# Kernel tuning notes

Measured on AMD Instinct MI355X. Metric: run time of the kernel, lower is better.

The kernel has to match this reference:

```python
import jax, jax.numpy as jnp
import numpy as np
from jax import lax

GAMMA = 1.5
ALPHA = 0.4
RADIUS = 2            # cv2 d=5 -> radius 2
SIGMA_COLOR = 0.05
SIGMA_SPACE = 50.0
BN_EPS = 1e-5


def setup_inputs() -> dict:
    key = jax.random.key(0)
    ks = jax.random.split(key, 6)
    B, C, H, W, F, L = 8, 1, 256, 256, 64, 15
    x = jax.random.normal(ks[0], (B, C, H, W), dtype=jnp.float32)
    w_init = jax.random.normal(ks[1], (F, C, 3, 3), dtype=jnp.float32) * 0.05
    w_body = jax.random.normal(ks[2], (L, F, F, 3, 3), dtype=jnp.float32) * 0.05
    bn_gamma = jnp.ones((L, F), dtype=jnp.float32) + 0.1 * jax.random.normal(ks[3], (L, F), dtype=jnp.float32)
    bn_beta = 0.1 * jax.random.normal(ks[4], (L, F), dtype=jnp.float32)
    w_final = jax.random.normal(ks[5], (C, F, 3, 3), dtype=jnp.float32) * 0.05
    return {"x": x, "w_init": w_init, "w_body": w_body,
            "bn_gamma": bn_gamma, "bn_beta": bn_beta, "w_final": w_final}


def _bilateral(img):
    # img: [B, H, W]; 5x5 bilateral filter, reflect-101 borders (cv2 default)
    r = RADIUS
    H, W = img.shape[1], img.shape[2]
    p = jnp.pad(img, ((0, 0), (r, r), (r, r)), mode='reflect')
    inv2sc = 1.0 / (2.0 * SIGMA_COLOR * SIGMA_COLOR)
    inv2ss = 1.0 / (2.0 * SIGMA_SPACE * SIGMA_SPACE)
    num = jnp.zeros_like(img)
    den = jnp.zeros_like(img)
    for dy in range(-r, r + 1):
        for dx in range(-r, r + 1):
            nb = p[:, dy + r:dy + r + H, dx + r:dx + r + W]
            sw = np.exp(-(dy * dy + dx * dx) * (1.0 / (2.0 * SIGMA_SPACE ** 2)))
            w = sw * jnp.exp(-(nb - img) ** 2 * inv2sc)
            num = num + w * nb
            den = den + w
    return num / den


def _preprocess(x):
    # x: [B, 1, H, W] in [-1, 1] nominal range
    xn = jnp.clip((x + 1.0) * 0.5, 1e-6, 1.0)
    img = xn[:, 0]                              # [B, H, W]
    blended = (1.0 - ALPHA) * img + ALPHA * jnp.power(img, GAMMA)
    return _bilateral(blended)[:, None]         # [B, 1, H, W]


def _conv(h, w):
    return lax.conv_general_dilated(h, w, (1, 1), 'SAME',
                                    dimension_numbers=('NCHW', 'OIHW', 'NCHW'))


def _dncnn(x_pre, w_init, w_body, bn_gamma, bn_beta, w_final):
    h = jax.nn.relu(_conv(x_pre, w_init))

    def body(h, params):
        w, g, b = params
        h = jax.nn.relu(_conv(h, w))
        mean = jnp.mean(h, axis=(0, 2, 3))
        var = jnp.var(h, axis=(0, 2, 3))
        h = (h - mean[None, :, None, None]) * jax.lax.rsqrt(var + BN_EPS)[None, :, None, None]
        h = h * g[None, :, None, None] + b[None, :, None, None]
        h = jax.nn.relu(h)
        return h, None

    h, _ = lax.scan(body, h, (w_body, bn_gamma, bn_beta))
    noise = _conv(h, w_final)
    return x_pre - noise


def reference(x, w_init, w_body, bn_gamma, bn_beta, w_final):
    x_pre = _preprocess(x)
    return _dncnn(x_pre, w_init, w_body, bn_gamma, bn_beta, w_final)
```

## Files before the change

kernel.cpp:

```cpp
#include <hip/hip_runtime.h>
#include <math.h>

#define B_   8
#define CH   64
#define H_   256
#define W_   256
#define NPIX (H_*W_)
#define NIMG (B_*NPIX)
#define NBLK 4096
#define PS   16

typedef short bf16x8 __attribute__((ext_vector_type(8)));
typedef float f32x4  __attribute__((ext_vector_type(4)));

__device__ float g_stats[256];
__device__ float g_part[128 * NBLK];
__device__ __align__(16) short g_wpk[15 * 18 * 4 * 64 * 16];

__device__ __forceinline__ int refl(int i) {
    if (i < 0)    return -i;
    if (i >= 256) return 510 - i;
    return i;
}
__device__ __forceinline__ float prep1(float v) {
    float xn = fminf(fmaxf((v + 1.0f) * 0.5f, 1e-6f), 1.0f);
    return 0.6f * xn + 0.4f * xn * sqrtf(xn);
}
__device__ __forceinline__ unsigned short bf16_rne(float f) {
    union { float f; unsigned u; } v; v.f = f;
    unsigned r = v.u + 0x7FFFu + ((v.u >> 16) & 1u);
    return (unsigned short)(r >> 16);
}
__device__ __forceinline__ float bf16_f(unsigned short h) {
    union { float f; unsigned u; } v; v.u = ((unsigned)h) << 16;
    return v.f;
}
__device__ __forceinline__ unsigned cvt_pk_bf16(float a, float b) {
    unsigned r;
    asm volatile("v_cvt_pk_bf16_f32 %0, %1, %2" : "=v"(r) : "v"(a), "v"(b));
    return r;
}
__device__ __forceinline__ void bar_lds() {
    asm volatile("s_waitcnt lgkmcnt(0)" ::: "memory");
    __builtin_amdgcn_s_barrier();
}

__global__ void init_ab_kernel() {
    int c = threadIdx.x;
    g_stats[128 + c] = 1.0f;
    g_stats[192 + c] = 0.0f;
}

__global__ void prepack_kernel(const float* __restrict__ w_body) {
    int idx = blockIdx.x * 256 + threadIdx.x;
    if (idx >= 15*18*4*64) return;
    int lane = idx & 63;
    int m    = (idx >> 6) & 3;
    int r2   = idx >> 8;
    int l    = r2 / 18;
    int s    = r2 - l * 18;
    int t  = s >> 1;
    int oc = m * 16 + (lane & 15);
    int icb = (s & 1) * 32 + (lane >> 4) * 8;
    union { short s[8]; int4 v; } uh, ul;
    #pragma unroll
    for (int j = 0; j < 8; ++j) {
        float w = w_body[(((size_t)l * 64 + oc) * 64 + (icb + j)) * 9 + t];
        unsigned short h = bf16_rne(w);
        unsigned short lo = bf16_rne(w - bf16_f(h));
        uh.s[j] = (short)h;
        ul.s[j] = (short)lo;
    }
    int4* dst = (int4*)(g_wpk + (size_t)idx * 16);
    dst[0] = uh.v;
    dst[1] = ul.v;
}

__global__ __launch_bounds__(256) void conv_init_kernel(
    const float* __restrict__ x, const float* __restrict__ wi,
    float* __restrict__ h)
{
    __shared__ float s_bl[14][38];
    __shared__ float s_xp[10][34];
    __shared__ float s_w[64 * 12];
    int bx = blockIdx.x, by = blockIdx.y, b = blockIdx.z;
    int tid = threadIdx.x;
    const float* xb = x + b * NPIX;

    for (int i = tid; i < 14*38; i += 256) {
        int r = i / 38, c = i - r * 38;
        int gy = refl(by * 8 + r - 3), gx = refl(bx * 32 + c - 3);
        s_bl[r][c] = prep1(xb[gy * W_ + gx]);
    }
    for (int i = tid; i < 576; i += 256) {
        int oc = i / 9, t = i - oc * 9;
        s_w[oc * 12 + t] = wi[i];
    }
    __syncthreads();

    for (int i = tid; i < 10*34; i += 256) {
        int r = i / 34, c = i - r * 34;
        int gy = by * 8 + r - 1, gx = bx * 32 + c - 1;
        float v = 0.f;
        if (gy >= 0 && gy < H_ && gx >= 0 && gx < W_) {
            float ctr = s_bl[r + 2][c + 2];
            float num = 0.f, den = 0.f;
            #pragma unroll
            for (int dy = -2; dy <= 2; ++dy)
                #pragma unroll
                for (int dx = -2; dx <= 2; ++dx) {
                    float nb = s_bl[r + 2 + dy][c + 2 + dx];
                    float d  = nb - ctr;
                    float wgt = expf(-(float)(dy*dy + dx*dx) * 2e-4f - d * d * 200.0f);
                    num += wgt * nb;
                    den += wgt;
                }
            v = num / den;
        }
        s_xp[r][c] = v;
    }
    __syncthreads();

    int px = tid & 31, py = tid >> 5;
    float v[9];
    #pragma unroll
    for (int dr = 0; dr < 3; ++dr)
        #pragma unroll
        for (int dc = 0; dc < 3; ++dc)
            v[dr*3+dc] = s_xp[py + dr][px + dc];

    float acc[64];
    #pragma unroll
    for (int oc = 0; oc < 64; ++oc) {
        f32x4 w0 = *(const f32x4*)&s_w[oc * 12];
        f32x4 w1 = *(const f32x4*)&s_w[oc * 12 + 4];
        float w8 = s_w[oc * 12 + 8];
        float a = w0[0]*v[0] + w0[1]*v[1] + w0[2]*v[2] + w0[3]*v[3];
        a += w1[0]*v[4] + w1[1]*v[5] + w1[2]*v[6] + w1[3]*v[7];
        a = fmaf(w8, v[8], a);
        acc[oc] = fmaxf(a, 0.f);
    }

    int gy = by * 8 + py, gx = bx * 32 + px;
    float* outp = h + ((size_t)(b * NPIX + gy * W_ + gx)) * 64;
    #pragma unroll
    for (int c4 = 0; c4 < 16; ++c4) {
        float4 o = make_float4(acc[4*c4], acc[4*c4+1], acc[4*c4+2], acc[4*c4+3]);
        *reinterpret_cast<float4*>(outp + 4*c4) = o;
    }
}

__global__ __launch_bounds__(256, 4) void conv_body_mfma(
    const float* __restrict__ hin, int l, float* __restrict__ hout)
{
    __shared__ unsigned s_hi[180 * PS];
    __shared__ unsigned s_lo[180 * PS];

    int tid  = threadIdx.x;
    int lane = tid & 63;
    int wv   = tid >> 6;

    int bid = blockIdx.x;
    int swz = (bid & 7) * 512 + (bid >> 3);
    int bx = swz & 15;
    int by = (swz >> 4) & 31;
    int b  = swz >> 9;

    const float* ab = &g_stats[128];
    int q   = tid & 7;
    int c0  = q * 4;
    int pr0 = tid >> 3;

    f32x4 acc[4][2];
    #pragma unroll
    for (int m = 0; m < 4; ++m)
        #pragma unroll
        for (int n = 0; n < 2; ++n)
            acc[m][n] = (f32x4){0.f, 0.f, 0.f, 0.f};

    auto split_store = [&](int p, float v0, float v1, float v2, float v3) {
        unsigned hh0 = cvt_pk_bf16(v0, v1);
        unsigned hh1 = cvt_pk_bf16(v2, v3);
        float f0 = __uint_as_float(hh0 << 16);
        float f1 = __uint_as_float(hh0 & 0xffff0000u);
        float f2 = __uint_as_float(hh1 << 16);
        float f3 = __uint_as_float(hh1 & 0xffff0000u);
        unsigned ll0 = cvt_pk_bf16(v0 - f0, v1 - f1);
        unsigned ll1 = cvt_pk_bf16(v2 - f2, v3 - f3);
        *(uint2*)&s_hi[p * PS + 2*q] = make_uint2(hh0, hh1);
        *(uint2*)&s_lo[p * PS + 2*q] = make_uint2(ll0, ll1);
    };

    auto stage_safe = [&](int chunk) {
        float4 a4 = *(const float4*)&ab[chunk * 32 + c0];
        float4 b4 = *(const float4*)&ab[64 + chunk * 32 + c0];
        #pragma unroll
        for (int k = 0; k < 6; ++k) {
            int p = k * 32 + pr0;
            if (p < 180) {
                int y = p / 18, xx = p - y * 18;
                int gy = by * 8 + y - 1, gx = bx * 16 + xx - 1;
                bool inb = (gy >= 0 && gy < H_ && gx >= 0 && gx < W_);
                const float4* src = (const float4*)(
                    hin + ((size_t)(b * NPIX + (inb ? gy * W_ + gx : 0))) * 64 + chunk * 32 + c0);
                float4 v = *src;
                float v0 = inb ? fmaxf(fmaf(v.x, a4.x, b4.x), 0.f) : 0.f;
                float v1 = inb ? fmaxf(fmaf(v.y, a4.y, b4.y), 0.f) : 0.f;
                float v2 = inb ? fmaxf(fmaf(v.z, a4.z, b4.z), 0.f) : 0.f;
                float v3 = inb ? fmaxf(fmaf(v.w, a4.w, b4.w), 0.f) : 0.f;
                split_store(p, v0, v1, v2, v3);
            }
        }
    };

    auto stage_fast = [&](int chunk) {
        float4 a4 = *(const float4*)&ab[chunk * 32 + c0];
        float4 b4 = *(const float4*)&ab[64 + chunk * 32 + c0];
        const float* hbase = hin
            + ((size_t)(b * NPIX + (by * 8 - 1) * W_ + (bx * 16 - 1))) * 64
            + chunk * 32 + c0;
        #pragma unroll
        for (int k = 0; k < 6; ++k) {
            int p = k * 32 + pr0;
            if (p < 180) {
                int y = p / 18, xx = p - y * 18;
                float4 v = *(const float4*)(hbase + ((size_t)(y * W_ + xx)) * 64);
                float v0 = fmaxf(fmaf(v.x, a4.x, b4.x), 0.f);
                float v1 = fmaxf(fmaf(v.y, a4.y, b4.y), 0.f);
                float v2 = fmaxf(fmaf(v.z, a4.z, b4.z), 0.f);
                float v3 = fmaxf(fmaf(v.w, a4.w, b4.w), 0.f);
                split_store(p, v0, v1, v2, v3);
            }
        }
    };

    bool interior = (bx >= 1 && bx <= 14 && by >= 1 && by <= 30);

    auto compute_chunk = [&](int chunk) {
        __builtin_amdgcn_s_setprio(1);
        #pragma unroll
        for (int t = 0; t < 9; ++t) {
            int s = 2 * t + chunk;
            const short* wb = g_wpk + ((size_t)(((l * 18 + s) * 4) * 64 + lane)) * 16;
            bf16x8 a_hi[4], a_lo[4];
            #pragma unroll
            for (int m = 0; m < 4; ++m) {
                const short* pw = wb + (size_t)m * 1024;
                a_hi[m] = *(const bf16x8*)(pw);
                a_lo[m] = *(const bf16x8*)(pw + 8);
            }
            int dr = t / 3, dc = t - dr * 3;
            #pragma unroll
            for (int n = 0; n < 2; ++n) {
                int y = 2 * wv + n + dr;
                int p = y * 18 + dc + (lane & 15);
                int woff = p * PS + (lane >> 4) * 4;
                bf16x8 b_hi = *(const bf16x8*)&s_hi[woff];
                bf16x8 b_lo = *(const bf16x8*)&s_lo[woff];
                #pragma unroll
                for (int m = 0; m < 4; ++m) {
                    acc[m][n] = __builtin_amdgcn_mfma_f32_16x16x32_bf16(a_hi[m], b_hi, acc[m][n], 0, 0, 0);
                    acc[m][n] = __builtin_amdgcn_mfma_f32_16x16x32_bf16(a_hi[m], b_lo, acc[m][n], 0, 0, 0);
                    acc[m][n] = __builtin_amdgcn_mfma_f32_16x16x32_bf16(a_lo[m], b_hi, acc[m][n], 0, 0, 0);
                }
            }
        }
        __builtin_amdgcn_s_setprio(0);
    };

    int ck0 = (bid >> 8) & 1;
    if (interior) stage_fast(ck0); else stage_safe(ck0);
    bar_lds();
    compute_chunk(ck0);
    bar_lds();
    if (interior) stage_fast(ck0 ^ 1); else stage_safe(ck0 ^ 1);
    bar_lds();
    compute_chunk(ck0 ^ 1);

    bar_lds();
    float* s_red = (float*)s_hi;

    int q4  = lane >> 4;
    int gxs = bx * 16 + (lane & 15);
    float ps1[4][4], ps2[4][4];
    #pragma unroll
    for (int m = 0; m < 4; ++m)
        #pragma unroll
        for (int r = 0; r < 4; ++r) { ps1[m][r] = 0.f; ps2[m][r] = 0.f; }

    #pragma unroll
    for (int n = 0; n < 2; ++n) {
        int gy = by * 8 + 2 * wv + n;
        float* op = hout + ((size_t)(b * NPIX + gy * W_ + gxs)) * 64 + q4 * 4;
        #pragma unroll
        for (int m = 0; m < 4; ++m) {
            float a0 = fmaxf(acc[m][n][0], 0.f);
            float a1 = fmaxf(acc[m][n][1], 0.f);
            float a2 = fmaxf(acc[m][n][2], 0.f);
            float a3 = fmaxf(acc[m][n][3], 0.f);
            *reinterpret_cast<float4*>(op + m * 16) = make_float4(a0, a1, a2, a3);
            ps1[m][0] += a0; ps1[m][1] += a1; ps1[m][2] += a2; ps1[m][3] += a3;
            ps2[m][0] += a0*a0; ps2[m][1] += a1*a1; ps2[m][2] += a2*a2; ps2[m][3] += a3*a3;
        }
    }
    #pragma unroll
    for (int m = 0; m < 4; ++m) {
        #pragma unroll
        for (int r = 0; r < 4; ++r) {
            float a = ps1[m][r], s = ps2[m][r];
            #pragma unroll
            for (int off = 1; off < 16; off <<= 1) {
                a += __shfl_xor(a, off);
                s += __shfl_xor(s, off);
            }
            if ((lane & 15) == 0) {
                int oc = m * 16 + q4 * 4 + r;
                s_red[(wv * 64 + oc) * 2]     = a;
                s_red[(wv * 64 + oc) * 2 + 1] = s;
            }
        }
    }
    __syncthreads();
    if (tid < 128) {
        float v = s_red[tid] + s_red[128 + tid] + s_red[256 + tid] + s_red[384 + tid];
        g_part[(size_t)tid * NBLK + bid] = v;
    }
}

__global__ __launch_bounds__(256) void bn_finalize_kernel(
    const float* __restrict__ gamma, const float* __restrict__ beta)
{
    __shared__ float s[8];
    int c = blockIdx.x;
    int t = threadIdx.x;
    const float* p1 = g_part + (size_t)(2 * c) * NBLK;
    const float* p2 = g_part + (size_t)(2 * c + 1) * NBLK;
    float s1 = 0.f, s2 = 0.f;
    for (int i = t; i < NBLK; i += 256) { s1 += p1[i]; s2 += p2[i]; }
    #pragma unroll
    for (int off = 32; off >= 1; off >>= 1) {
        s1 += __shfl_xor(s1, off);
        s2 += __shfl_xor(s2, off);
    }
    int lane = t & 63, w = t >> 6;
    if (lane == 0) { s[w * 2] = s1; s[w * 2 + 1] = s2; }
    __syncthreads();
    if (t == 0) {
        float sum = s[0] + s[2] + s[4] + s[6];
        float sq  = s[1] + s[3] + s[5] + s[7];
        const float invN = 1.0f / (float)NIMG;
        float mean = sum * invN;
        float var  = sq * invN - mean * mean;
        float a = gamma[c] / sqrtf(var + 1e-5f);
        g_stats[128 + c] = a;
        g_stats[192 + c] = beta[c] - mean * a;
    }
}

__global__ __launch_bounds__(256) void conv_final_kernel(
    const float* __restrict__ hin, const float* __restrict__ wf,
    const float* __restrict__ x, float* __restrict__ out)
{
    __shared__ float s_in[324 * 36];
    __shared__ float s_bl[20][21];
    __shared__ float s_w[64 * 12];
    int bx = blockIdx.x, by = blockIdx.y, b = blockIdx.z;
    int tid = threadIdx.x;
    const float* xb = x + b * NPIX;
    const float* ab = &g_stats[128];

    for (int i = tid; i < 20*20; i += 256) {
        int r = i / 20, c = i - r * 20;
        int gy = refl(by * 16 + r - 2), gx = refl(bx * 16 + c - 2);
        s_bl[r][c] = prep1(xb[gy * W_ + gx]);
    }
    for (int i = tid; i < 576; i += 256) {
        int ic = i / 9, t = i - ic * 9;
        s_w[ic * 12 + t] = wf[i];
    }
    __syncthreads();

    int px = tid & 15, py = tid >> 4;
    float ctr = s_bl[py + 2][px + 2];
    float num = 0.f, den = 0.f;
    #pragma unroll
    for (int dy = -2; dy <= 2; ++dy)
        #pragma unroll
        for (int dx = -2; dx <= 2; ++dx) {
            float nb = s_bl[py + 2 + dy][px + 2 + dx];
            float d  = nb - ctr;
            float wgt = expf(-(float)(dy*dy + dx*dx) * 2e-4f - d * d * 200.0f);
            num += wgt * nb;
            den += wgt;
        }
    float xpre = num / den;

    int q   = tid & 7;
    int c0  = q * 4;
    int pr0 = tid >> 3;
    float acc = 0.f;

    for (int chunk = 0; chunk < 2; ++chunk) {
        __syncthreads();
        float4 a4 = *(const float4*)&ab[chunk * 32 + c0];
        float4 b4 = *(const float4*)&ab[64 + chunk * 32 + c0];
        #pragma unroll
        for (int k = 0; k < 11; ++k) {
            int p = k * 32 + pr0;
            if (p < 324) {
                int y = p / 18, xx = p - y * 18;
                int gy = by * 16 + y - 1, gx = bx * 16 + xx - 1;
                bool inb = (gy >= 0 && gy < H_ && gx >= 0 && gx < W_);
                const float4* src = (const float4*)(
                    hin + ((size_t)(b * NPIX + (inb ? gy * W_ + gx : 0))) * 64 + chunk * 32 + c0);
                float4 v = *src;
                float4 o;
                o.x = inb ? fmaxf(fmaf(v.x, a4.x, b4.x), 0.f) : 0.f;
                o.y = inb ? fmaxf(fmaf(v.y, a4.y, b4.y), 0.f) : 0.f;
                o.z = inb ? fmaxf(fmaf(v.z, a4.z, b4.z), 0.f) : 0.f;
                o.w = inb ? fmaxf(fmaf(v.w, a4.w, b4.w), 0.f) : 0.f;
                *(float4*)&s_in[p * 36 + 4*q] = o;
            }
        }
        __syncthreads();

        #pragma unroll
        for (int u = 0; u < 8; ++u) {
            f32x4 wreg[4][3];
            #pragma unroll
            for (int e = 0; e < 4; ++e)
                #pragma unroll
                for (int g = 0; g < 3; ++g)
                    wreg[e][g] = *(const f32x4*)&s_w[(chunk * 32 + u * 4 + e) * 12 + g * 4];
            #pragma unroll
            for (int t = 0; t < 9; ++t) {
                int dr = t / 3, dc = t - dr * 3;
                const float4 hv = *(const float4*)&s_in[((py + dr) * 18 + px + dc) * 36 + 4 * u];
                acc = fmaf(hv.x, wreg[0][t >> 2][t & 3], acc);
                acc = fmaf(hv.y, wreg[1][t >> 2][t & 3], acc);
                acc = fmaf(hv.z, wreg[2][t >> 2][t & 3], acc);
                acc = fmaf(hv.w, wreg[3][t >> 2][t & 3], acc);
            }
        }
    }

    int gy = by * 16 + py, gx = bx * 16 + px;
    out[b * NPIX + gy * W_ + gx] = xpre - acc;
}

extern "C" void kernel_launch(void* const* d_in, const int* in_sizes, int n_in,
                              void* d_out, int out_size, void* d_ws, size_t ws_size,
                              hipStream_t stream)
{
    const float* x        = (const float*)d_in[0];
    const float* w_init   = (const float*)d_in[1];
    const float* w_body   = (const float*)d_in[2];
    const float* bn_gamma = (const float*)d_in[3];
    const float* bn_beta  = (const float*)d_in[4];
    const float* w_final  = (const float*)d_in[5];
    float* out = (float*)d_out;

    char* wsb = (char*)d_ws;
    float* hA = (float*)wsb;
    float* hB = (float*)(wsb + 134217728ULL);

    init_ab_kernel <<<1, 64, 0, stream>>>();
    prepack_kernel <<<270, 256, 0, stream>>>(w_body);
    conv_init_kernel<<<dim3(8, 32, 8), 256, 0, stream>>>(x, w_init, hA);

    float* cur = hA;
    float* nxt = hB;
    for (int l = 0; l < 15; ++l) {
        conv_body_mfma<<<NBLK, 256, 0, stream>>>(cur, l, nxt);
        bn_finalize_kernel<<<64, 256, 0, stream>>>(bn_gamma + l * 64, bn_beta + l * 64);
        float* tp = cur; cur = nxt; nxt = tp;
    }
    conv_final_kernel<<<dim3(16, 16, 8), 256, 0, stream>>>(cur, w_final, x, out);
}
```

Before: 2.139 ms.

## Switch body conv MFMA from 16x16x32 to 32x32x16 tiles

```diff
diff --git a/kernel.cpp b/kernel.cpp
--- a/kernel.cpp
+++ b/kernel.cpp
@@ -12,10 +12,11 @@
 
 typedef short bf16x8 __attribute__((ext_vector_type(8)));
 typedef float f32x4  __attribute__((ext_vector_type(4)));
+typedef float f32x16 __attribute__((ext_vector_type(16)));
 
 __device__ float g_stats[256];
 __device__ float g_part[128 * NBLK];
-__device__ __align__(16) short g_wpk[15 * 18 * 4 * 64 * 16];
+__device__ __align__(16) short g_wpk[15 * 36 * 2 * 64 * 16];
 
 __device__ __forceinline__ int refl(int i) {
     if (i < 0)    return -i;
@@ -53,15 +54,16 @@
 
 __global__ void prepack_kernel(const float* __restrict__ w_body) {
     int idx = blockIdx.x * 256 + threadIdx.x;
-    if (idx >= 15*18*4*64) return;
+    if (idx >= 15*36*2*64) return;
     int lane = idx & 63;
-    int m    = (idx >> 6) & 3;
-    int r2   = idx >> 8;
-    int l    = r2 / 18;
-    int s    = r2 - l * 18;
-    int t  = s >> 1;
-    int oc = m * 16 + (lane & 15);
-    int icb = (s & 1) * 32 + (lane >> 4) * 8;
+    int mt   = (idx >> 6) & 1;
+    int r2   = idx >> 7;
+    int l    = r2 / 36;
+    int ss   = r2 - l * 36;
+    int t   = ss >> 2;
+    int icq = ss & 3;
+    int oc  = mt * 32 + (lane & 31);
+    int icb = icq * 16 + (lane >> 5) * 8;
     union { short s[8]; int4 v; } uh, ul;
     #pragma unroll
     for (int j = 0; j < 8; ++j) {
@@ -171,12 +173,9 @@
     int c0  = q * 4;
     int pr0 = tid >> 3;
 
-    f32x4 acc[4][2];
-    #pragma unroll
-    for (int m = 0; m < 4; ++m)
-        #pragma unroll
-        for (int n = 0; n < 2; ++n)
-            acc[m][n] = (f32x4){0.f, 0.f, 0.f, 0.f};
+    f32x16 acc2[2];
+    acc2[0] = (f32x16){0.f,0.f,0.f,0.f,0.f,0.f,0.f,0.f,0.f,0.f,0.f,0.f,0.f,0.f,0.f,0.f};
+    acc2[1] = acc2[0];
 
     auto split_store = [&](int p, float v0, float v1, float v2, float v3) {
         unsigned hh0 = cvt_pk_bf16(v0, v1);
@@ -240,29 +239,25 @@
         __builtin_amdgcn_s_setprio(1);
         #pragma unroll
         for (int t = 0; t < 9; ++t) {
-            int s = 2 * t + chunk;
-            const short* wb = g_wpk + ((size_t)(((l * 18 + s) * 4) * 64 + lane)) * 16;
-            bf16x8 a_hi[4], a_lo[4];
+            int dr = t / 3, dc = t - dr * 3;
+            int pbase = (2 * wv + ((lane & 31) >> 4) + dr) * 18 + (lane & 15) + dc;
             #pragma unroll
-            for (int m = 0; m < 4; ++m) {
-                const short* pw = wb + (size_t)m * 1024;
-                a_hi[m] = *(const bf16x8*)(pw);
-                a_lo[m] = *(const bf16x8*)(pw + 8);
-            }
-            int dr = t / 3, dc = t - dr * 3;
-            #pragma unroll
-            for (int n = 0; n < 2; ++n) {
-                int y = 2 * wv + n + dr;
-                int p = y * 18 + dc + (lane & 15);
-                int woff = p * PS + (lane >> 4) * 4;
-                bf16x8 b_hi = *(const bf16x8*)&s_hi[woff];
-                bf16x8 b_lo = *(const bf16x8*)&s_lo[woff];
-                #pragma unroll
-                for (int m = 0; m < 4; ++m) {
-                    acc[m][n] = __builtin_amdgcn_mfma_f32_16x16x32_bf16(a_hi[m], b_hi, acc[m][n], 0, 0, 0);
-                    acc[m][n] = __builtin_amdgcn_mfma_f32_16x16x32_bf16(a_hi[m], b_lo, acc[m][n], 0, 0, 0);
-                    acc[m][n] = __builtin_amdgcn_mfma_f32_16x16x32_bf16(a_lo[m], b_hi, acc[m][n], 0, 0, 0);
-                }
+            for (int s16 = 0; s16 < 2; ++s16) {
+                int ss = t * 4 + chunk * 2 + s16;
+                const short* wb = g_wpk + ((size_t)((l * 36 + ss) * 2) * 64 + lane) * 16;
+                bf16x8 a0h = *(const bf16x8*)(wb);
+                bf16x8 a0l = *(const bf16x8*)(wb + 8);
+                bf16x8 a1h = *(const bf16x8*)(wb + 1024);
+                bf16x8 a1l = *(const bf16x8*)(wb + 1024 + 8);
+                int woff = pbase * PS + s16 * 8 + (lane >> 5) * 4;
+                bf16x8 bh = *(const bf16x8*)&s_hi[woff];
+                bf16x8 bl = *(const bf16x8*)&s_lo[woff];
+                acc2[0] = __builtin_amdgcn_mfma_f32_32x32x16_bf16(a0h, bh, acc2[0], 0, 0, 0);
+                acc2[0] = __builtin_amdgcn_mfma_f32_32x32x16_bf16(a0h, bl, acc2[0], 0, 0, 0);
+                acc2[0] = __builtin_amdgcn_mfma_f32_32x32x16_bf16(a0l, bh, acc2[0], 0, 0, 0);
+                acc2[1] = __builtin_amdgcn_mfma_f32_32x32x16_bf16(a1h, bh, acc2[1], 0, 0, 0);
+                acc2[1] = __builtin_amdgcn_mfma_f32_32x32x16_bf16(a1h, bl, acc2[1], 0, 0, 0);
+                acc2[1] = __builtin_amdgcn_mfma_f32_32x32x16_bf16(a1l, bh, acc2[1], 0, 0, 0);
             }
         }
         __builtin_amdgcn_s_setprio(0);
@@ -280,43 +275,35 @@
     bar_lds();
     float* s_red = (float*)s_hi;
 
-    int q4  = lane >> 4;
-    int gxs = bx * 16 + (lane & 15);
-    float ps1[4][4], ps2[4][4];
-    #pragma unroll
-    for (int m = 0; m < 4; ++m)
-        #pragma unroll
-        for (int r = 0; r < 4; ++r) { ps1[m][r] = 0.f; ps2[m][r] = 0.f; }
-
-    #pragma unroll
-    for (int n = 0; n < 2; ++n) {
-        int gy = by * 8 + 2 * wv + n;
-        float* op = hout + ((size_t)(b * NPIX + gy * W_ + gxs)) * 64 + q4 * 4;
-        #pragma unroll
-        for (int m = 0; m < 4; ++m) {
-            float a0 = fmaxf(acc[m][n][0], 0.f);
-            float a1 = fmaxf(acc[m][n][1], 0.f);
-            float a2 = fmaxf(acc[m][n][2], 0.f);
-            float a3 = fmaxf(acc[m][n][3], 0.f);
-            *reinterpret_cast<float4*>(op + m * 16) = make_float4(a0, a1, a2, a3);
-            ps1[m][0] += a0; ps1[m][1] += a1; ps1[m][2] += a2; ps1[m][3] += a3;
-            ps2[m][0] += a0*a0; ps2[m][1] += a1*a1; ps2[m][2] += a2*a2; ps2[m][3] += a3*a3;
-        }
-    }
-    #pragma unroll
-    for (int m = 0; m < 4; ++m) {
-        #pragma unroll
-        for (int r = 0; r < 4; ++r) {
-            float a = ps1[m][r], s = ps2[m][r];
+    int colp = lane & 31;
+    int gy = by * 8 + 2 * wv + (colp >> 4);
+    int gx = bx * 16 + (colp & 15);
+    float* op = hout + ((size_t)(b * NPIX + gy * W_ + gx)) * 64;
+    int hi4 = (lane >> 5) * 4;
+
+    #pragma unroll
+    for (int mt = 0; mt < 2; ++mt) {
+        #pragma unroll
+        for (int a = 0; a < 4; ++a) {
+            float v0 = fmaxf(acc2[mt][4*a + 0], 0.f);
+            float v1 = fmaxf(acc2[mt][4*a + 1], 0.f);
+            float v2 = fmaxf(acc2[mt][4*a + 2], 0.f);
+            float v3 = fmaxf(acc2[mt][4*a + 3], 0.f);
+            int oc0 = mt * 32 + 8 * a + hi4;
+            *reinterpret_cast<float4*>(op + oc0) = make_float4(v0, v1, v2, v3);
             #pragma unroll
-            for (int off = 1; off < 16; off <<= 1) {
-                a += __shfl_xor(a, off);
-                s += __shfl_xor(s, off);
-            }
-            if ((lane & 15) == 0) {
-                int oc = m * 16 + q4 * 4 + r;
-                s_red[(wv * 64 + oc) * 2]     = a;
-                s_red[(wv * 64 + oc) * 2 + 1] = s;
+            for (int rr = 0; rr < 4; ++rr) {
+                float s = (rr == 0) ? v0 : (rr == 1) ? v1 : (rr == 2) ? v2 : v3;
+                float qq = s * s;
+                #pragma unroll
+                for (int off = 1; off < 32; off <<= 1) {
+                    s  += __shfl_xor(s,  off);
+                    qq += __shfl_xor(qq, off);
+                }
+                if (colp == 0) {
+                    s_red[(wv * 64 + oc0 + rr) * 2]     = s;
+                    s_red[(wv * 64 + oc0 + rr) * 2 + 1] = qq;
+                }
             }
         }
     }
```

New measurement: 2.564 ms. +19.9%, slower.
